# Performance work log

Measured on AMD Instinct MI355X. Metric: run time of the kernel, lower is better.

## Reference

```python
import jax, jax.numpy as jnp
import numpy as np

D = 512
H = 8
HD = D // H
EPS = 1e-8


def setup_inputs() -> dict:
    key = jax.random.key(0)
    ks = jax.random.split(key, 16)
    B, S = 4, 2048
    s = lambda n: 1.0 / np.sqrt(n)
    inp = {
        "gene_emb": jax.random.normal(ks[0], (B, S, D), jnp.float32),
        "expr_emb": jax.random.normal(ks[1], (B, S, D), jnp.float32),
        "M": jax.random.uniform(ks[2], (B, S, S), jnp.float32),
        # weights stored (in, out) so y = x @ W + b
        "W_fused": jax.random.normal(ks[3], (2 * D, D), jnp.float32) * s(2 * D),
        "b_fused": jnp.zeros((D,), jnp.float32),
        "W_Q": jax.random.normal(ks[4], (D, D), jnp.float32) * s(D),
        "b_Q": jnp.zeros((D,), jnp.float32),
        "W_K": jax.random.normal(ks[5], (D, D), jnp.float32) * s(D),
        "b_K": jnp.zeros((D,), jnp.float32),
        "W_V": jax.random.normal(ks[6], (D, D), jnp.float32) * s(D),
        "b_V": jnp.zeros((D,), jnp.float32),
        "W_O": jax.random.normal(ks[7], (D, D), jnp.float32) * s(D),
        "b_O": jnp.zeros((D,), jnp.float32),
    }
    return inp


def reference(gene_emb, expr_emb, M, W_fused, b_fused, W_Q, b_Q, W_K, b_K, W_V, b_V, W_O, b_O):
    B, S, _ = gene_emb.shape
    scale = HD ** (-0.5)
    fused = jnp.concatenate([gene_emb, expr_emb], axis=-1) @ W_fused + b_fused
    # (B,S,D) -> (B,H,S,HD)
    split = lambda x: x.reshape(B, S, H, HD).transpose(0, 2, 1, 3)
    Q = split(fused @ W_Q + b_Q)
    K = split(fused @ W_K + b_K)
    V = split(expr_emb @ W_V + b_V)
    scores = jnp.einsum("bhqd,bhkd->bhqk", Q, K) * scale
    Mg = M[:, None, :, :]  # broadcast over heads
    scores = scores * Mg
    attn = jax.nn.softmax(scores, axis=-1)
    A_sparse = attn * Mg
    norm = jnp.sum(jnp.abs(A_sparse), axis=-1, keepdims=True) + EPS
    A_bar = A_sparse / norm
    out = jnp.einsum("bhqk,bhkd->bhqd", A_bar, V)
    out = out.transpose(0, 2, 1, 3).reshape(B, S, D)
    return out @ W_O + b_O
```

## Files before the change

### kernel.cpp

```cpp
#include <hip/hip_runtime.h>

typedef unsigned short u16;
typedef __attribute__((ext_vector_type(8))) short bf16x8_t;
typedef __attribute__((ext_vector_type(4))) float f32x4_t;

__device__ __forceinline__ u16 f2bf(float x){
  union { float f; unsigned u; } v; v.f = x;
  unsigned r = v.u + 0x7FFFu + ((v.u >> 16) & 1u);
  return (u16)(r >> 16);
}
__device__ __forceinline__ float bf2f(u16 h){
  union { unsigned u; float f; } v; v.u = ((unsigned)h) << 16;
  return v.f;
}
__device__ __forceinline__ u16 hi16(float x){
  union { float f; unsigned u; } v; v.f = x;
  return (u16)(v.u >> 16);
}

__device__ __forceinline__ void gl2lds16(const u16* g, u16* l){
  __builtin_amdgcn_global_load_lds((const __attribute__((address_space(1))) void*)g,
                                   (__attribute__((address_space(3))) void*)l, 16, 0, 0);
}

__global__ __launch_bounds__(256) void split_concat_kernel(
    const float* __restrict__ gene, const float* __restrict__ expr,
    u16* __restrict__ Xh, u16* __restrict__ Xl)
{
  size_t e = ((size_t)blockIdx.x * 256 + threadIdx.x) * 4;
  int row = (int)(e >> 10);
  int col = (int)(e & 1023);
  const float* src = (col < 512) ? (gene + (size_t)row * 512 + col)
                                 : (expr + (size_t)row * 512 + (col - 512));
  float4 v = *(const float4*)src;
  float a[4] = {v.x, v.y, v.z, v.w};
  u16 hs[4], ls[4];
#pragma unroll
  for (int i = 0; i < 4; i++){
    hs[i] = f2bf(a[i]);
    ls[i] = f2bf(a[i] - bf2f(hs[i]));
  }
  *(uint2*)(Xh + e) = make_uint2(hs[0] | ((unsigned)hs[1] << 16), hs[2] | ((unsigned)hs[3] << 16));
  *(uint2*)(Xl + e) = make_uint2(ls[0] | ((unsigned)ls[1] << 16), ls[2] | ((unsigned)ls[3] << 16));
}

__global__ __launch_bounds__(256) void transpose_all_kernel(
    const float* __restrict__ Wf, const float* __restrict__ Wq,
    const float* __restrict__ Wk, const float* __restrict__ Wv,
    const float* __restrict__ Wo,
    u16* __restrict__ Wfth, u16* __restrict__ Wftl,
    u16* __restrict__ Wqth, u16* __restrict__ Wkth,
    u16* __restrict__ Wvth, u16* __restrict__ Woth)
{
  __shared__ float t[64][65];
  int id = blockIdx.x;
  const float* W; u16* Th; u16* Tl; int K, kx, ny;
  if (id < 128){ W = Wf; Th = Wfth; Tl = Wftl; K = 1024; kx = id >> 3; ny = id & 7; }
  else {
    int tt = id - 128; int wi = tt >> 6; tt &= 63; kx = tt >> 3; ny = tt & 7; K = 512;
    W  = (wi == 0) ? Wq  : (wi == 1) ? Wk  : (wi == 2) ? Wv  : Wo;
    Th = (wi == 0) ? Wqth: (wi == 1) ? Wkth: (wi == 2) ? Wvth: Woth;
    Tl = nullptr;
  }
  int k0 = kx * 64, n0 = ny * 64;
  int tid = threadIdx.x;
  int r = tid >> 4;
  int c4 = (tid & 15) * 4;
#pragma unroll
  for (int p = 0; p < 4; p++){
    int k = p * 16 + r;
    float4 v = *(const float4*)(W + (size_t)(k0 + k) * 512 + n0 + c4);
    t[c4 + 0][k] = v.x; t[c4 + 1][k] = v.y; t[c4 + 2][k] = v.z; t[c4 + 3][k] = v.w;
  }
  __syncthreads();
#pragma unroll
  for (int p = 0; p < 4; p++){
    int n = p * 16 + r;
    u16 hs[4], ls[4];
#pragma unroll
    for (int i = 0; i < 4; i++){
      float x = t[n][c4 + i];
      hs[i] = f2bf(x);
      ls[i] = f2bf(x - bf2f(hs[i]));
    }
    size_t o = (size_t)(n0 + n) * K + k0 + c4;
    *(uint2*)(Th + o) = make_uint2(hs[0] | ((unsigned)hs[1] << 16), hs[2] | ((unsigned)hs[3] << 16));
    if (Tl)
      *(uint2*)(Tl + o) = make_uint2(ls[0] | ((unsigned)ls[1] << 16), ls[2] | ((unsigned)ls[3] << 16));
  }
}

template<int SPLITS, int MODE, int DUAL>
__global__ __launch_bounds__(256, 2) void gemm_kernel(
    const u16* __restrict__ Ah, const u16* __restrict__ Al, int lda,
    const u16* __restrict__ Bh0, const u16* __restrict__ Bl0,
    const u16* __restrict__ Bh1, int K,
    const float* __restrict__ bias0, const float* __restrict__ bias1,
    void* __restrict__ out0, void* __restrict__ out1, void* __restrict__ outsec,
    float sc0, float sc1)
{
  __shared__ __align__(16) u16 sAh[128 * 32];
  __shared__ __align__(16) u16 sAl[SPLITS >= 2 ? 128 * 32 : 8];
  __shared__ __align__(16) u16 sBh[64 * 32];
  __shared__ __align__(16) u16 sBl[SPLITS == 3 ? 64 * 32 : 8];
  int tid = threadIdx.x;
  int lane = tid & 63, w = tid >> 6, quad = lane >> 4, l15 = lane & 15;
  int wm = w & 1, wn = w >> 1;
  int m0 = blockIdx.x * 128;
  int side = DUAL ? (int)(blockIdx.y >> 3) : 0;
  int n0 = (DUAL ? (int)(blockIdx.y & 7) : (int)blockIdx.y) * 64;
  const u16* Bh = (DUAL && side) ? Bh1 : Bh0;
  const float* bias = (DUAL && side) ? bias1 : bias0;
  void* o0 = (DUAL && side) ? outsec : out0;
  float sc = (DUAL && side) ? sc1 : sc0;

  f32x4_t acc[4][2];
#pragma unroll
  for (int i = 0; i < 4; i++)
#pragma unroll
    for (int j = 0; j < 2; j++)
#pragma unroll
      for (int r = 0; r < 4; r++) acc[i][j][r] = 0.f;

  int lrow = lane >> 2;
  int swzS = ((lane >> 2) & 3) ^ ((lane >> 4) & 3);
  int gkq  = ((lane & 3) ^ swzS) * 8;
  const u16* pAh0 = Ah + (size_t)(m0 + w * 32 + lrow) * lda + gkq;
  const u16* pAh1 = Ah + (size_t)(m0 + w * 32 + 16 + lrow) * lda + gkq;
  const u16* pAl0 = (SPLITS >= 2) ? Al + (size_t)(m0 + w * 32 + lrow) * lda + gkq : nullptr;
  const u16* pAl1 = (SPLITS >= 2) ? Al + (size_t)(m0 + w * 32 + 16 + lrow) * lda + gkq : nullptr;
  const u16* pBh0 = Bh + (size_t)(n0 + w * 16 + lrow) * K + gkq;
  const u16* pBl0 = (SPLITS == 3) ? Bl0 + (size_t)(n0 + w * 16 + lrow) * K + gkq : nullptr;
  u16* dAh = sAh + w * 1024;
  u16* dAl = sAl + w * 1024;
  u16* dBh = sBh + w * 512;
  u16* dBl = sBl + w * 512;

  int pq = (quad ^ ((l15 & 3) ^ ((l15 >> 2) & 3))) * 8;

  for (int k0 = 0; k0 < K; k0 += 32){
    __syncthreads();
    gl2lds16(pAh0 + k0, dAh);
    gl2lds16(pAh1 + k0, dAh + 512);
    if constexpr (SPLITS >= 2){
      gl2lds16(pAl0 + k0, dAl);
      gl2lds16(pAl1 + k0, dAl + 512);
    }
    gl2lds16(pBh0 + k0, dBh);
    if constexpr (SPLITS == 3)
      gl2lds16(pBl0 + k0, dBl);
    __syncthreads();

    bf16x8_t aH[4], aL[4], bH[2], bL[2];
#pragma unroll
    for (int mi = 0; mi < 4; mi++){
      int ad = (wm * 64 + mi * 16 + l15) * 32 + pq;
      aH[mi] = *(const bf16x8_t*)&sAh[ad];
      if constexpr (SPLITS >= 2) aL[mi] = *(const bf16x8_t*)&sAl[ad];
    }
#pragma unroll
    for (int ni = 0; ni < 2; ni++){
      int bd = (wn * 32 + ni * 16 + l15) * 32 + pq;
      bH[ni] = *(const bf16x8_t*)&sBh[bd];
      if constexpr (SPLITS == 3) bL[ni] = *(const bf16x8_t*)&sBl[bd];
    }
#pragma unroll
    for (int mi = 0; mi < 4; mi++)
#pragma unroll
      for (int ni = 0; ni < 2; ni++){
        acc[mi][ni] = __builtin_amdgcn_mfma_f32_16x16x32_bf16(aH[mi], bH[ni], acc[mi][ni], 0, 0, 0);
        if constexpr (SPLITS == 3)
          acc[mi][ni] = __builtin_amdgcn_mfma_f32_16x16x32_bf16(aH[mi], bL[ni], acc[mi][ni], 0, 0, 0);
        if constexpr (SPLITS >= 2)
          acc[mi][ni] = __builtin_amdgcn_mfma_f32_16x16x32_bf16(aL[mi], bH[ni], acc[mi][ni], 0, 0, 0);
      }
  }

#pragma unroll
  for (int mi = 0; mi < 4; mi++)
#pragma unroll
    for (int ni = 0; ni < 2; ni++){
      int gn = n0 + wn * 32 + ni * 16 + l15;
      float bs = bias[gn];
      int gm0 = m0 + wm * 64 + mi * 16 + quad * 4;
#pragma unroll
      for (int r = 0; r < 4; r++){
        float v = acc[mi][ni][r] + bs;
        int gm = gm0 + r;
        if constexpr (MODE == 0){
          u16 hb = f2bf(v);
          ((u16*)o0)[(size_t)gm * 512 + gn] = hb;
          ((u16*)out1)[(size_t)gm * 512 + gn] = f2bf(v - bf2f(hb));
        } else if constexpr (MODE == 1){
          ((u16*)o0)[(size_t)gm * 512 + gn] = f2bf(v * sc);
        } else if constexpr (MODE == 2){
          int bb = gm >> 11, s = gm & 2047;
          int hh = gn >> 6, d = gn & 63;
          ((u16*)o0)[((size_t)((bb * 8 + hh) * 64 + d) << 11) + s] = f2bf(v);
        } else {
          ((float*)o0)[(size_t)gm * 512 + gn] = v;
        }
      }
    }
}

__global__ __launch_bounds__(256, 4) void flash_kernel(
    const u16* __restrict__ Qh, const u16* __restrict__ Kh,
    const u16* __restrict__ Vt, const float* __restrict__ Mm,
    u16* __restrict__ Oh)
{
  __shared__ __align__(16) u16 sKh[64 * 64], sVt[64 * 64];
  __shared__ __align__(16) u16 sP[64 * 72];
  int tid = threadIdx.x, lane = tid & 63, w = tid >> 6, quad = lane >> 4, l15 = lane & 15;
  int bh = blockIdx.y, b = bh >> 3, h = bh & 7;
  int q0 = blockIdx.x * 64;

  int qrow = q0 + w * 16 + l15;
  const u16* qp = Qh + ((size_t)(b * 2048 + qrow)) * 512 + h * 64 + quad * 8;
  bf16x8_t qH[2];
  qH[0] = *(const bf16x8_t*)qp;  qH[1] = *(const bf16x8_t*)(qp + 32);

  float lp[4] = {0.f, 0.f, 0.f, 0.f};
  f32x4_t Oacc[4];
#pragma unroll
  for (int ni = 0; ni < 4; ni++)
#pragma unroll
    for (int r = 0; r < 4; r++) Oacc[ni][r] = 0.f;

  int srow = lane >> 3;
  int gc = ((lane & 7) ^ ((lane >> 3) & 7)) * 8;
  const u16* gKh0 = Kh + ((size_t)(b * 2048 + w * 16 + srow)) * 512 + h * 64 + gc;
  const u16* gVt0 = Vt + ((size_t)(bh * 64 + w * 16 + srow)) * 2048 + gc;
  u16* dKh = sKh + w * 1024;
  u16* dVt = sVt + w * 1024;
  const float* Mbase = Mm + (size_t)b * 2048 * 2048 + (size_t)(q0 + w * 16) * 2048;

  float Mc[4][4];
#pragma unroll
  for (int ni = 0; ni < 4; ni++)
#pragma unroll
    for (int r = 0; r < 4; r++)
      Mc[ni][r] = Mbase[(size_t)(quad * 4 + r) * 2048 + ni * 16 + l15];

  int sw7 = l15 & 7;
  for (int k0 = 0; k0 < 2048; k0 += 64){
    __syncthreads();
    gl2lds16(gKh0 + (size_t)k0 * 512,       dKh);
    gl2lds16(gKh0 + (size_t)(k0 + 8) * 512, dKh + 512);
    gl2lds16(gVt0 + k0,                     dVt);
    gl2lds16(gVt0 + 8 * 2048 + k0,          dVt + 512);
    __syncthreads();

    float Mn[4][4];
    bool hasNext = (k0 + 64) < 2048;
    if (hasNext){
#pragma unroll
      for (int ni = 0; ni < 4; ni++)
#pragma unroll
        for (int r = 0; r < 4; r++)
          Mn[ni][r] = Mbase[(size_t)(quad * 4 + r) * 2048 + (k0 + 64) + ni * 16 + l15];
    }

    f32x4_t Sacc[4];
#pragma unroll
    for (int ni = 0; ni < 4; ni++)
#pragma unroll
      for (int r = 0; r < 4; r++) Sacc[ni][r] = 0.f;
#pragma unroll
    for (int ni = 0; ni < 4; ni++){
      int kb = (ni * 16 + l15) * 64;
#pragma unroll
      for (int ds = 0; ds < 2; ds++){
        int p = ((ds * 4 + quad) ^ sw7) * 8;
        bf16x8_t kH = *(const bf16x8_t*)&sKh[kb + p];
        Sacc[ni] = __builtin_amdgcn_mfma_f32_16x16x32_bf16(qH[ds], kH, Sacc[ni], 0, 0, 0);
      }
    }

#pragma unroll
    for (int ni = 0; ni < 4; ni++)
#pragma unroll
      for (int r = 0; r < 4; r++){
        float m = Mc[ni][r];
        float p = m * __builtin_amdgcn_exp2f(Sacc[ni][r] * m);
        lp[r] += p;
        sP[(w * 16 + quad * 4 + r) * 72 + ni * 16 + l15] = hi16(p);
      }

#pragma unroll
    for (int ds = 0; ds < 2; ds++){
      bf16x8_t pf = *(const bf16x8_t*)&sP[(w * 16 + l15) * 72 + ds * 32 + quad * 8];
#pragma unroll
      for (int ni = 0; ni < 4; ni++){
        int p = ((ds * 4 + quad) ^ sw7) * 8;
        bf16x8_t vf = *(const bf16x8_t*)&sVt[(ni * 16 + l15) * 64 + p];
        Oacc[ni] = __builtin_amdgcn_mfma_f32_16x16x32_bf16(pf, vf, Oacc[ni], 0, 0, 0);
      }
    }

    if (hasNext){
#pragma unroll
      for (int ni = 0; ni < 4; ni++)
#pragma unroll
        for (int r = 0; r < 4; r++) Mc[ni][r] = Mn[ni][r];
    }
  }

#pragma unroll
  for (int r = 0; r < 4; r++){
#pragma unroll
    for (int off = 1; off < 16; off <<= 1)
      lp[r] += __shfl_xor(lp[r], off);
  }

#pragma unroll
  for (int r = 0; r < 4; r++){
    float inv = 1.0f / lp[r];
    int q = q0 + w * 16 + quad * 4 + r;
    size_t rb = ((size_t)(b * 2048 + q)) * 512 + h * 64;
#pragma unroll
    for (int ni = 0; ni < 4; ni++){
      float v = Oacc[ni][r] * inv;
      Oh[rb + ni * 16 + l15] = f2bf(v);
    }
  }
}

extern "C" void kernel_launch(void* const* d_in, const int* in_sizes, int n_in,
                              void* d_out, int out_size, void* d_ws, size_t ws_size,
                              hipStream_t stream)
{
  const float* gene = (const float*)d_in[0];
  const float* expr = (const float*)d_in[1];
  const float* Mm   = (const float*)d_in[2];
  const float* Wf   = (const float*)d_in[3];
  const float* bfv  = (const float*)d_in[4];
  const float* Wq   = (const float*)d_in[5];
  const float* bq   = (const float*)d_in[6];
  const float* Wk   = (const float*)d_in[7];
  const float* bk   = (const float*)d_in[8];
  const float* Wv   = (const float*)d_in[9];
  const float* bv   = (const float*)d_in[10];
  const float* Wo   = (const float*)d_in[11];
  const float* bo   = (const float*)d_in[12];
  float* out = (float*)d_out;

  char* ws = (char*)d_ws;
  size_t off = 0;
  auto alloc = [&](size_t bytes) -> void* {
    void* p = (void*)(ws + off);
    off += (bytes + 255) & ~(size_t)255;
    return p;
  };
  u16* Xh   = (u16*)alloc(8192ull * 1024 * 2);
  u16* Xl   = (u16*)alloc(8192ull * 1024 * 2);
  u16* Wfth = (u16*)alloc(512ull * 1024 * 2);
  u16* Wftl = (u16*)alloc(512ull * 1024 * 2);
  u16* Wqth = (u16*)alloc(512ull * 512 * 2);
  u16* Wkth = (u16*)alloc(512ull * 512 * 2);
  u16* Wvth = (u16*)alloc(512ull * 512 * 2);
  u16* Woth = (u16*)alloc(512ull * 512 * 2);
  u16* Fh   = (u16*)alloc(8192ull * 512 * 2);
  u16* Fl   = (u16*)alloc(8192ull * 512 * 2);
  u16* Qh   = (u16*)alloc(8192ull * 512 * 2);
  u16* Kh   = (u16*)alloc(8192ull * 512 * 2);
  u16* Vt   = (u16*)alloc(8192ull * 512 * 2);
  u16* Oh = Xh;

  const float QSC = 0.1803368801f;

  split_concat_kernel<<<8192, 256, 0, stream>>>(gene, expr, Xh, Xl);
  transpose_all_kernel<<<384, 256, 0, stream>>>(Wf, Wq, Wk, Wv, Wo,
                                                Wfth, Wftl, Wqth, Wkth, Wvth, Woth);

  gemm_kernel<3, 0, 0><<<dim3(64, 8), 256, 0, stream>>>(
      Xh, Xl, 1024, Wfth, Wftl, nullptr, 1024, bfv, nullptr, Fh, Fl, nullptr, 1.f, 1.f);
  gemm_kernel<2, 1, 1><<<dim3(64, 16), 256, 0, stream>>>(
      Fh, Fl, 512, Wqth, nullptr, Wkth, 512, bq, bk, Qh, nullptr, Kh, QSC, 1.f);
  gemm_kernel<2, 2, 0><<<dim3(64, 8), 256, 0, stream>>>(
      Xh + 512, Xl + 512, 1024, Wvth, nullptr, nullptr, 512, bv, nullptr, Vt, nullptr, nullptr, 1.f, 1.f);
  flash_kernel<<<dim3(32, 32), 256, 0, stream>>>(Qh, Kh, Vt, Mm, Oh);
  gemm_kernel<1, 3, 0><<<dim3(64, 8), 256, 0, stream>>>(
      Oh, nullptr, 512, Woth, nullptr, nullptr, 512, bo, nullptr, out, nullptr, nullptr, 1.f, 1.f);

  (void)in_sizes; (void)n_in; (void)out_size; (void)ws_size;
}
```

Before: 299.8 us.

## Compute transposed S=K·Q^T in flash kernel to keep P in registers, drop LDS

The flash kernel now computes the score tile with K as the A operand and Q as the B operand, so each lane holds probabilities for consecutive keys of one query. These are packed straight into the bf16 B operand of the PV MFMA, which removes the shared-memory round trip for P and all K/V LDS staging and barriers. K and V fragments are now loaded directly from global memory into registers, and the mask is read with vectorized float4 loads. The grid is reordered with head outermost so that blocks of the same head share K/V in L2, and launch bounds drop to 2 blocks per SM. The cost is more global/L2 traffic for K/V, since each wave reloads them without LDS sharing, plus higher register pressure.

```diff
diff --git a/kernel.cpp b/kernel.cpp
--- a/kernel.cpp
+++ b/kernel.cpp
@@ -13,9 +13,9 @@
   union { unsigned u; float f; } v; v.u = ((unsigned)h) << 16;
   return v.f;
 }
-__device__ __forceinline__ u16 hi16(float x){
-  union { float f; unsigned u; } v; v.f = x;
-  return (u16)(v.u >> 16);
+__device__ __forceinline__ unsigned pack_hi16(float a, float b){
+  union { float f; unsigned u; } x, y; x.f = a; y.f = b;
+  return (x.u >> 16) | (y.u & 0xFFFF0000u);
 }
 
 __device__ __forceinline__ void gl2lds16(const u16* g, u16* l){
@@ -204,125 +204,123 @@
     }
 }
 
-__global__ __launch_bounds__(256, 4) void flash_kernel(
+__global__ __launch_bounds__(256, 2) void flash_kernel(
     const u16* __restrict__ Qh, const u16* __restrict__ Kh,
     const u16* __restrict__ Vt, const float* __restrict__ Mm,
     u16* __restrict__ Oh)
 {
-  __shared__ __align__(16) u16 sKh[64 * 64], sVt[64 * 64];
-  __shared__ __align__(16) u16 sP[64 * 72];
   int tid = threadIdx.x, lane = tid & 63, w = tid >> 6, quad = lane >> 4, l15 = lane & 15;
-  int bh = blockIdx.y, b = bh >> 3, h = bh & 7;
-  int q0 = blockIdx.x * 64;
-
-  int qrow = q0 + w * 16 + l15;
-  const u16* qp = Qh + ((size_t)(b * 2048 + qrow)) * 512 + h * 64 + quad * 8;
+  int bid = blockIdx.x;
+  int h = bid >> 7, rem = bid & 127, b = rem & 3, q0 = (rem >> 2) * 64;
+  int q = q0 + w * 16 + l15;
+
+  const u16* qp = Qh + ((size_t)(b * 2048 + q)) * 512 + h * 64 + quad * 8;
   bf16x8_t qH[2];
-  qH[0] = *(const bf16x8_t*)qp;  qH[1] = *(const bf16x8_t*)(qp + 32);
-
-  float lp[4] = {0.f, 0.f, 0.f, 0.f};
+  qH[0] = *(const bf16x8_t*)qp;
+  qH[1] = *(const bf16x8_t*)(qp + 32);
+
+  int krowb = ((l15 >> 2) << 3) + (l15 & 3);
+  const u16* kp = Kh + ((size_t)(b * 2048 + krowb)) * 512 + h * 64 + quad * 8;
+  const u16* vp = Vt + ((size_t)((b * 8 + h) * 64 + l15)) * 2048 + quad * 8;
+  const float* mp = Mm + (size_t)b * (2048 * 2048) + (size_t)q * 2048 + quad * 8;
+
+  float lp = 0.f;
   f32x4_t Oacc[4];
 #pragma unroll
-  for (int ni = 0; ni < 4; ni++)
-#pragma unroll
-    for (int r = 0; r < 4; r++) Oacc[ni][r] = 0.f;
-
-  int srow = lane >> 3;
-  int gc = ((lane & 7) ^ ((lane >> 3) & 7)) * 8;
-  const u16* gKh0 = Kh + ((size_t)(b * 2048 + w * 16 + srow)) * 512 + h * 64 + gc;
-  const u16* gVt0 = Vt + ((size_t)(bh * 64 + w * 16 + srow)) * 2048 + gc;
-  u16* dKh = sKh + w * 1024;
-  u16* dVt = sVt + w * 1024;
-  const float* Mbase = Mm + (size_t)b * 2048 * 2048 + (size_t)(q0 + w * 16) * 2048;
-
-  float Mc[4][4];
-#pragma unroll
-  for (int ni = 0; ni < 4; ni++)
-#pragma unroll
-    for (int r = 0; r < 4; r++)
-      Mc[ni][r] = Mbase[(size_t)(quad * 4 + r) * 2048 + ni * 16 + l15];
-
-  int sw7 = l15 & 7;
+  for (int dn = 0; dn < 4; dn++)
+#pragma unroll
+    for (int r = 0; r < 4; r++) Oacc[dn][r] = 0.f;
+
+  f32x4_t Mc[2][2];
+#pragma unroll
+  for (int pt = 0; pt < 2; pt++)
+#pragma unroll
+    for (int t = 0; t < 2; t++)
+      Mc[pt][t] = *(const f32x4_t*)(mp + pt * 32 + t * 4);
+
   for (int k0 = 0; k0 < 2048; k0 += 64){
-    __syncthreads();
-    gl2lds16(gKh0 + (size_t)k0 * 512,       dKh);
-    gl2lds16(gKh0 + (size_t)(k0 + 8) * 512, dKh + 512);
-    gl2lds16(gVt0 + k0,                     dVt);
-    gl2lds16(gVt0 + 8 * 2048 + k0,          dVt + 512);
-    __syncthreads();
-
-    float Mn[4][4];
+    const u16* kpk = kp + (size_t)k0 * 512;
+    const u16* vpk = vp + k0;
+
+    bf16x8_t kf[2][2][2];
+#pragma unroll
+    for (int pt = 0; pt < 2; pt++)
+#pragma unroll
+      for (int t = 0; t < 2; t++)
+#pragma unroll
+        for (int ds = 0; ds < 2; ds++)
+          kf[pt][t][ds] = *(const bf16x8_t*)(kpk + (size_t)(pt * 32 + t * 4) * 512 + ds * 32);
+
+    bf16x8_t vf[4][2];
+#pragma unroll
+    for (int dn = 0; dn < 4; dn++)
+#pragma unroll
+      for (int pt = 0; pt < 2; pt++)
+        vf[dn][pt] = *(const bf16x8_t*)(vpk + (size_t)dn * (16 * 2048) + pt * 32);
+
+    f32x4_t Mn[2][2];
     bool hasNext = (k0 + 64) < 2048;
     if (hasNext){
 #pragma unroll
-      for (int ni = 0; ni < 4; ni++)
-#pragma unroll
-        for (int r = 0; r < 4; r++)
-          Mn[ni][r] = Mbase[(size_t)(quad * 4 + r) * 2048 + (k0 + 64) + ni * 16 + l15];
-    }
-
-    f32x4_t Sacc[4];
-#pragma unroll
-    for (int ni = 0; ni < 4; ni++)
-#pragma unroll
-      for (int r = 0; r < 4; r++) Sacc[ni][r] = 0.f;
-#pragma unroll
-    for (int ni = 0; ni < 4; ni++){
-      int kb = (ni * 16 + l15) * 64;
-#pragma unroll
-      for (int ds = 0; ds < 2; ds++){
-        int p = ((ds * 4 + quad) ^ sw7) * 8;
-        bf16x8_t kH = *(const bf16x8_t*)&sKh[kb + p];
-        Sacc[ni] = __builtin_amdgcn_mfma_f32_16x16x32_bf16(qH[ds], kH, Sacc[ni], 0, 0, 0);
+      for (int pt = 0; pt < 2; pt++)
+#pragma unroll
+        for (int t = 0; t < 2; t++)
+          Mn[pt][t] = *(const f32x4_t*)(mp + (k0 + 64) + pt * 32 + t * 4);
+    }
+
+    f32x4_t S[2][2];
+#pragma unroll
+    for (int pt = 0; pt < 2; pt++)
+#pragma unroll
+      for (int t = 0; t < 2; t++){
+        f32x4_t s;
+#pragma unroll
+        for (int r = 0; r < 4; r++) s[r] = 0.f;
+        s = __builtin_amdgcn_mfma_f32_16x16x32_bf16(kf[pt][t][0], qH[0], s, 0, 0, 0);
+        s = __builtin_amdgcn_mfma_f32_16x16x32_bf16(kf[pt][t][1], qH[1], s, 0, 0, 0);
+        S[pt][t] = s;
       }
-    }
-
-#pragma unroll
-    for (int ni = 0; ni < 4; ni++)
-#pragma unroll
-      for (int r = 0; r < 4; r++){
-        float m = Mc[ni][r];
-        float p = m * __builtin_amdgcn_exp2f(Sacc[ni][r] * m);
-        lp[r] += p;
-        sP[(w * 16 + quad * 4 + r) * 72 + ni * 16 + l15] = hi16(p);
-      }
-
-#pragma unroll
-    for (int ds = 0; ds < 2; ds++){
-      bf16x8_t pf = *(const bf16x8_t*)&sP[(w * 16 + l15) * 72 + ds * 32 + quad * 8];
-#pragma unroll
-      for (int ni = 0; ni < 4; ni++){
-        int p = ((ds * 4 + quad) ^ sw7) * 8;
-        bf16x8_t vf = *(const bf16x8_t*)&sVt[(ni * 16 + l15) * 64 + p];
-        Oacc[ni] = __builtin_amdgcn_mfma_f32_16x16x32_bf16(pf, vf, Oacc[ni], 0, 0, 0);
-      }
+
+#pragma unroll
+    for (int pt = 0; pt < 2; pt++){
+      float p[2][4];
+#pragma unroll
+      for (int t = 0; t < 2; t++)
+#pragma unroll
+        for (int r = 0; r < 4; r++){
+          float m = Mc[pt][t][r];
+          float v = m * __builtin_amdgcn_exp2f(S[pt][t][r] * m);
+          lp += v;
+          p[t][r] = v;
+        }
+      union { unsigned u[4]; bf16x8_t v8; } pb;
+      pb.u[0] = pack_hi16(p[0][0], p[0][1]);
+      pb.u[1] = pack_hi16(p[0][2], p[0][3]);
+      pb.u[2] = pack_hi16(p[1][0], p[1][1]);
+      pb.u[3] = pack_hi16(p[1][2], p[1][3]);
+#pragma unroll
+      for (int dn = 0; dn < 4; dn++)
+        Oacc[dn] = __builtin_amdgcn_mfma_f32_16x16x32_bf16(vf[dn][pt], pb.v8, Oacc[dn], 0, 0, 0);
     }
 
     if (hasNext){
 #pragma unroll
-      for (int ni = 0; ni < 4; ni++)
-#pragma unroll
-        for (int r = 0; r < 4; r++) Mc[ni][r] = Mn[ni][r];
-    }
-  }
-
-#pragma unroll
-  for (int r = 0; r < 4; r++){
-#pragma unroll
-    for (int off = 1; off < 16; off <<= 1)
-      lp[r] += __shfl_xor(lp[r], off);
-  }
-
-#pragma unroll
-  for (int r = 0; r < 4; r++){
-    float inv = 1.0f / lp[r];
-    int q = q0 + w * 16 + quad * 4 + r;
-    size_t rb = ((size_t)(b * 2048 + q)) * 512 + h * 64;
-#pragma unroll
-    for (int ni = 0; ni < 4; ni++){
-      float v = Oacc[ni][r] * inv;
-      Oh[rb + ni * 16 + l15] = f2bf(v);
-    }
+      for (int pt = 0; pt < 2; pt++)
+#pragma unroll
+        for (int t = 0; t < 2; t++) Mc[pt][t] = Mn[pt][t];
+    }
+  }
+
+  lp += __shfl_xor(lp, 16);
+  lp += __shfl_xor(lp, 32);
+  float inv = 1.0f / lp;
+
+  size_t ob = ((size_t)(b * 2048 + q)) * 512 + h * 64 + quad * 4;
+#pragma unroll
+  for (int dn = 0; dn < 4; dn++){
+    unsigned w0 = (unsigned)f2bf(Oacc[dn][0] * inv) | ((unsigned)f2bf(Oacc[dn][1] * inv) << 16);
+    unsigned w1 = (unsigned)f2bf(Oacc[dn][2] * inv) | ((unsigned)f2bf(Oacc[dn][3] * inv) << 16);
+    *(uint2*)(Oh + ob + dn * 16) = make_uint2(w0, w1);
   }
 }
 
@@ -379,7 +377,7 @@
       Fh, Fl, 512, Wqth, nullptr, Wkth, 512, bq, bk, Qh, nullptr, Kh, QSC, 1.f);
   gemm_kernel<2, 2, 0><<<dim3(64, 8), 256, 0, stream>>>(
       Xh + 512, Xl + 512, 1024, Wvth, nullptr, nullptr, 512, bv, nullptr, Vt, nullptr, nullptr, 1.f, 1.f);
-  flash_kernel<<<dim3(32, 32), 256, 0, stream>>>(Qh, Kh, Vt, Mm, Oh);
+  flash_kernel<<<1024, 256, 0, stream>>>(Qh, Kh, Vt, Mm, Oh);
   gemm_kernel<1, 3, 0><<<dim3(64, 8), 256, 0, stream>>>(
       Oh, nullptr, 512, Woth, nullptr, nullptr, 512, bo, nullptr, out, nullptr, nullptr, 1.f, 1.f);
 
```

After: 509.8 us. 70.1% more time.
